# Kernel optimization log

Measured on AMD Instinct MI355X. Metric: run time of the kernel, lower is better.

## Reference

```python
import jax, jax.numpy as jnp
import numpy as np

N = 50000      # nodes
E = 800000     # edges (avg degree 16)
DIN = 500      # input_dim
HID = 100      # hid_dim (fixed in module)
DOUT = 64      # output_dim
EPS = 1e-5     # LayerNorm eps (torch default)


def _layer_norm(x, g, b):
    mu = jnp.mean(x, axis=-1, keepdims=True)
    var = jnp.var(x, axis=-1, keepdims=True)
    return (x - mu) / jnp.sqrt(var + EPS) * g + b


def _gcn_conv(x, src, tgt, W, b):
    # PyG GCNConv: self-loops + symmetric normalization + linear + scatter-add
    h = x @ W  # [N, out]
    idx = jnp.arange(N)
    src_sl = jnp.concatenate([src, idx])
    tgt_sl = jnp.concatenate([tgt, idx])
    deg = jax.ops.segment_sum(jnp.ones(src_sl.shape, h.dtype), tgt_sl, num_segments=N)
    dinv = jnp.where(deg > 0, deg ** -0.5, 0.0)
    norm = dinv[src_sl] * dinv[tgt_sl]  # [E+N]
    out = jax.ops.segment_sum(h[src_sl] * norm[:, None], tgt_sl, num_segments=N)
    return out + b


def setup_inputs() -> dict:
    key = jax.random.key(0)
    ks = jax.random.split(key, 10)
    glorot = lambda k, fi, fo: jax.random.normal(k, (fi, fo), jnp.float32) * np.float32(1.0 / np.sqrt(fi))
    z = lambda d: jnp.zeros((d,), jnp.float32)
    return dict(
        data_x=jax.random.normal(ks[0], (N, DIN), jnp.float32),
        data_edge_index=jax.random.randint(ks[1], (2, E), 0, N),
        data_edge_attr=jnp.zeros((E,), jnp.int32),  # single relation type
        t_W1=glorot(ks[2], DIN, HID), t_b1=z(HID), t_g1=jnp.ones((HID,), jnp.float32), t_be1=z(HID),
        t_W2=glorot(ks[3], HID, HID), t_b2=z(HID), t_g2=jnp.ones((HID,), jnp.float32), t_be2=z(HID),
        r_Wrel=glorot(ks[4], HID, HID)[None],  # [n_relations=1, H, H]
        r_Wself=glorot(ks[5], HID, HID), r_b=z(HID),
        c1_W=glorot(ks[6], HID, HID), c1_b=z(HID),
        c2_W=glorot(ks[7], HID, DOUT), c2_b=z(DOUT),
    )


def reference(data_x, data_edge_index, data_edge_attr,
              t_W1, t_b1, t_g1, t_be1, t_W2, t_b2, t_g2, t_be2,
              r_Wrel, r_Wself, r_b, c1_W, c1_b, c2_W, c2_b):
    src, tgt = data_edge_index[0], data_edge_index[1]
    # transform: Linear -> LN -> ReLU -> Linear -> LN -> ReLU
    x = jax.nn.relu(_layer_norm(data_x @ t_W1 + t_b1, t_g1, t_be1))
    x = jax.nn.relu(_layer_norm(x @ t_W2 + t_b2, t_g2, t_be2))
    # RGCN, n_relations=1, n_layers=1: per-relation message + self transform
    msgs = x[src] @ r_Wrel[0]  # edge_attr is all relation 0
    x = x @ r_Wself + jax.ops.segment_sum(msgs, tgt, num_segments=N) + r_b
    x = jax.nn.relu(x)  # dropout = identity (eval)
    x = jax.nn.relu(_gcn_conv(x, src, tgt, c1_W, c1_b))
    x = _gcn_conv(x, src, tgt, c2_W, c2_b)
    return jax.nn.log_softmax(x, axis=1)
```

## Files before the change

kernel.cpp:

```cpp
#include <hip/hip_runtime.h>
#include <hip/hip_bf16.h>

typedef __attribute__((ext_vector_type(8))) short short8;
typedef __attribute__((ext_vector_type(8))) unsigned short ushort8;
typedef __attribute__((ext_vector_type(4))) float f32x4;

static constexpr int NN = 50000;
static constexpr int NE = 800000;
static constexpr int SCAN_B = 196;

#define MFMA16x16x32 __builtin_amdgcn_mfma_f32_16x16x32_bf16

__device__ __forceinline__ float b2f(unsigned short u){
  unsigned v = ((unsigned)u) << 16;
  return __builtin_bit_cast(float, v);
}
__device__ __forceinline__ unsigned short f2b(float f){
  unsigned x = __builtin_bit_cast(unsigned, f);
  unsigned r = (x + 0x7fffu + ((x >> 16) & 1u)) >> 16;
  return (unsigned short)r;
}

__device__ __align__(256) int   g_isf32;
__device__ __align__(256) unsigned short g_W1t  [112 * 512];
__device__ __align__(256) unsigned short g_W2t  [112 * 128];
__device__ __align__(256) unsigned short g_WselfT[112 * 128];
__device__ __align__(256) unsigned short g_WrelT [112 * 128];
__device__ __align__(256) unsigned short g_c1Wt [112 * 128];
__device__ __align__(256) unsigned short g_c2Wt [64 * 128];
__device__ __align__(256) unsigned short g_bufA[(size_t)NN * 128];
__device__ __align__(256) unsigned short g_bufB[(size_t)NN * 128];
__device__ __align__(256) unsigned short g_bufC[(size_t)NN * 128];
__device__ __align__(256) int   g_deg[NN];
__device__ __align__(256) int   g_rowptr[NN + 1];
__device__ __align__(256) int   g_cursor[NN];
__device__ __align__(256) int   g_colidx[NE];
__device__ __align__(256) float g_dinv[NN];
__device__ __align__(256) int   g_partial[256];

__device__ __forceinline__ float ld_in(const void* p, int idx, int isf32){
  if (isf32) return ((const float*)p)[idx];
  return b2f(((const unsigned short*)p)[idx]);
}

__global__ void k_detect(const unsigned short* __restrict__ x){
  __shared__ int sh[256];
  int tid = threadIdx.x;
  int cnt = 0;
  for (int j = 0; j < 16; j++){
    unsigned short h = x[(size_t)(tid * 16 + j) * 2];
    int e = (h >> 7) & 0xFF;
    if (e >= 90 && e <= 160) cnt++;
  }
  sh[tid] = cnt;
  __syncthreads();
  for (int off = 128; off > 0; off >>= 1){
    if (tid < off) sh[tid] += sh[tid + off];
    __syncthreads();
  }
  if (tid == 0) g_isf32 = (sh[0] < 2458) ? 1 : 0;
}

__global__ void k_zero(){
  int i = blockIdx.x * 256 + threadIdx.x;
  if (i < NN){ g_deg[i] = 0; g_cursor[i] = 0; }
}

__device__ __forceinline__ void xp_one(const void* W, unsigned short* Wt, int idx,
                                       int K, int Nc, int Kpad, int isf32){
  int n = idx / Kpad;
  int k = idx - n * Kpad;
  float v = 0.f;
  if (n < Nc && k < K) v = ld_in(W, k * Nc + n, isf32);
  Wt[idx] = f2b(v);
}
__global__ void k_transpose_all(const void* W1, const void* W2, const void* Wself,
                                const void* Wrel, const void* c1W, const void* c2W){
  int idx = blockIdx.x * 256 + threadIdx.x;
  const int isf32 = g_isf32;
  if (idx < 57344){ xp_one(W1, g_W1t, idx, 500, 100, 512, isf32); return; }
  idx -= 57344;
  if (idx < 14336){ xp_one(W2,    g_W2t,    idx, 100, 100, 128, isf32); return; }
  idx -= 14336;
  if (idx < 14336){ xp_one(Wself, g_WselfT, idx, 100, 100, 128, isf32); return; }
  idx -= 14336;
  if (idx < 14336){ xp_one(Wrel,  g_WrelT,  idx, 100, 100, 128, isf32); return; }
  idx -= 14336;
  if (idx < 14336){ xp_one(c1W,   g_c1Wt,   idx, 100, 100, 128, isf32); return; }
  idx -= 14336;
  if (idx < 8192){  xp_one(c2W,   g_c2Wt,   idx, 100, 64,  128, isf32); }
}

__global__ void k_deg(const int* __restrict__ tgt){
  int e = blockIdx.x * 256 + threadIdx.x;
  if (e < NE) atomicAdd(&g_deg[tgt[e]], 1);
}

__global__ __launch_bounds__(256) void k_scan1(){
  __shared__ int sh[256];
  int t = threadIdx.x;
  int i = blockIdx.x * 256 + t;
  int val = (i < NN) ? g_deg[i] : 0;
  sh[t] = val;
  __syncthreads();
#pragma unroll
  for (int off = 1; off < 256; off <<= 1){
    int v = (t >= off) ? sh[t - off] : 0;
    __syncthreads();
    sh[t] += v;
    __syncthreads();
  }
  if (i < NN){
    g_rowptr[i] = sh[t] - val;
    g_dinv[i] = rsqrtf((float)(val + 1));
  }
  if (t == 255) g_partial[blockIdx.x] = sh[255];
}
__global__ __launch_bounds__(256) void k_scan2(){
  __shared__ int sh[256];
  int t = threadIdx.x;
  int val = (t < SCAN_B) ? g_partial[t] : 0;
  sh[t] = val;
  __syncthreads();
#pragma unroll
  for (int off = 1; off < 256; off <<= 1){
    int v = (t >= off) ? sh[t - off] : 0;
    __syncthreads();
    sh[t] += v;
    __syncthreads();
  }
  if (t < SCAN_B) g_partial[t] = sh[t] - val;
  if (t == 255) g_rowptr[NN] = sh[255];
}
__global__ __launch_bounds__(256) void k_scan3(){
  int i = blockIdx.x * 256 + threadIdx.x;
  if (i < NN) g_rowptr[i] += g_partial[blockIdx.x];
}

__global__ void k_fill(const int* __restrict__ src, const int* __restrict__ tgt){
  int e = blockIdx.x * 256 + threadIdx.x;
  if (e >= NE) return;
  int t = tgt[e];
  int pos = g_rowptr[t] + atomicAdd(&g_cursor[t], 1);
  g_colidx[pos] = src[e];
}

template<int MODE>
__global__ __launch_bounds__(256) void k_agg(){
  const unsigned short* x = (MODE == 1) ? g_bufC : g_bufB;
  int node = blockIdx.x * 16 + (threadIdx.x >> 4);
  if (node >= NN) return;
  const int c8 = (threadIdx.x & 15) * 8;

  float wt = (MODE != 0) ? g_dinv[node] : 1.f;
  float a[4][8];
#pragma unroll
  for (int j = 0; j < 4; j++)
#pragma unroll
    for (int k = 0; k < 8; k++) a[j][k] = 0.f;

  int p0 = g_rowptr[node], p1 = g_rowptr[node + 1];
  for (int p = p0; p < p1; p += 4){
    int   sj[4]; float wj[4];
#pragma unroll
    for (int j = 0; j < 4; j++){
      bool ok = (p + j) < p1;
      sj[j] = ok ? g_colidx[p + j] : node;
      wj[j] = ok ? ((MODE != 0) ? g_dinv[sj[j]] * wt : 1.f) : 0.f;
    }
    ushort8 r[4];
#pragma unroll
    for (int j = 0; j < 4; j++)
      r[j] = *reinterpret_cast<const ushort8*>(&x[(size_t)sj[j] * 128 + c8]);
#pragma unroll
    for (int j = 0; j < 4; j++)
#pragma unroll
      for (int k = 0; k < 8; k++) a[j][k] += wj[j] * b2f((unsigned short)r[j][k]);
  }
  if (MODE != 0){
    float ws = wt * wt;
    ushort8 sv = *reinterpret_cast<const ushort8*>(&x[(size_t)node * 128 + c8]);
#pragma unroll
    for (int k = 0; k < 8; k++) a[0][k] += ws * b2f((unsigned short)sv[k]);
  }
  ushort8 o;
#pragma unroll
  for (int k = 0; k < 8; k++)
    o[k] = f2b(a[0][k] + a[1][k] + a[2][k] + a[3][k]);
  *reinterpret_cast<ushort8*>(&g_bufA[(size_t)node * 128 + c8]) = o;
}

__global__ __launch_bounds__(64, 1) void k_gemm1_ln(const void* __restrict__ Aext,
    const void* __restrict__ bias, const void* __restrict__ gamma,
    const void* __restrict__ beta){
  const int lane = threadIdx.x;
  const int m = lane & 15, q = lane >> 4;
  const int row0 = blockIdx.x * 16;
  const int isf32 = g_isf32;
  f32x4 acc[7] = {};

  if (isf32){
    const float* arow = (const float*)Aext + (size_t)(row0 + m) * 500;
    const int kq = q * 8;
    f32x4 lo = *reinterpret_cast<const f32x4*>(arow + min(kq, 496));
    f32x4 hi = *reinterpret_cast<const f32x4*>(arow + min(kq + 4, 496));
#pragma unroll
    for (int c = 0; c < 16; c++){
      f32x4 lo2 = lo, hi2 = hi;
      if (c < 15){
        int kn = (c + 1) * 32 + kq;
        lo2 = *reinterpret_cast<const f32x4*>(arow + min(kn, 496));
        hi2 = *reinterpret_cast<const f32x4*>(arow + min(kn + 4, 496));
      }
      short8 a = {(short)f2b(lo[0]), (short)f2b(lo[1]), (short)f2b(lo[2]), (short)f2b(lo[3]),
                  (short)f2b(hi[0]), (short)f2b(hi[1]), (short)f2b(hi[2]), (short)f2b(hi[3])};
      const int k0 = c * 32 + kq;
#pragma unroll
      for (int t = 0; t < 7; t++){
        short8 b = *reinterpret_cast<const short8*>(g_W1t + (size_t)(t * 16 + m) * 512 + k0);
        acc[t] = MFMA16x16x32(a, b, acc[t], 0, 0, 0);
      }
      lo = lo2; hi = hi2;
    }
  } else {
    const unsigned short* arow = (const unsigned short*)Aext + (size_t)(row0 + m) * 500;
    const int kq = q * 8;
    ushort4 lo = *reinterpret_cast<const ushort4*>(arow + min(kq, 496));
    ushort4 hi = *reinterpret_cast<const ushort4*>(arow + min(kq + 4, 496));
#pragma unroll
    for (int c = 0; c < 16; c++){
      ushort4 lo2 = lo, hi2 = hi;
      if (c < 15){
        int kn = (c + 1) * 32 + kq;
        lo2 = *reinterpret_cast<const ushort4*>(arow + min(kn, 496));
        hi2 = *reinterpret_cast<const ushort4*>(arow + min(kn + 4, 496));
      }
      short8 a = {(short)lo.x, (short)lo.y, (short)lo.z, (short)lo.w,
                  (short)hi.x, (short)hi.y, (short)hi.z, (short)hi.w};
      const int k0 = c * 32 + kq;
#pragma unroll
      for (int t = 0; t < 7; t++){
        short8 b = *reinterpret_cast<const short8*>(g_W1t + (size_t)(t * 16 + m) * 512 + k0);
        acc[t] = MFMA16x16x32(a, b, acc[t], 0, 0, 0);
      }
      lo = lo2; hi = hi2;
    }
  }

  float bf_[7], gf_[7], ef_[7];
#pragma unroll
  for (int t = 0; t < 7; t++){
    int col = t * 16 + m;
    bool ok = col < 100;
    bf_[t] = ok ? ld_in(bias, col, isf32)  : 0.f;
    gf_[t] = ok ? ld_in(gamma, col, isf32) : 0.f;
    ef_[t] = ok ? ld_in(beta, col, isf32)  : 0.f;
  }
#pragma unroll
  for (int r = 0; r < 4; r++){
    float vals[7], s1 = 0.f, s2 = 0.f;
#pragma unroll
    for (int t = 0; t < 7; t++){
      int col = t * 16 + m;
      float v = (col < 100) ? (acc[t][r] + bf_[t]) : 0.f;
      vals[t] = v; s1 += v; s2 += v * v;
    }
#pragma unroll
    for (int msk = 1; msk < 16; msk <<= 1){
      s1 += __shfl_xor(s1, msk, 64);
      s2 += __shfl_xor(s2, msk, 64);
    }
    float mu = s1 * 0.01f;
    float var = fmaxf(s2 * 0.01f - mu * mu, 0.f);
    float rstd = rsqrtf(var + 1e-5f);
    unsigned short* orow = g_bufA + (size_t)(row0 + q * 4 + r) * 128;
#pragma unroll
    for (int t = 0; t < 7; t++){
      int col = t * 16 + m;
      float y = fmaxf((vals[t] - mu) * rstd * gf_[t] + ef_[t], 0.f);
      orow[col] = f2b((col < 100) ? y : 0.f);
    }
    orow[112 + m] = 0;
  }
}

__global__ __launch_bounds__(256) void k_gemm2_ln(const void* __restrict__ bias,
    const void* __restrict__ gamma, const void* __restrict__ beta){
  const int isf32 = g_isf32;
  const int wave = threadIdx.x >> 6, lane = threadIdx.x & 63;
  const int m = lane & 15, q = lane >> 4;
  const int row0 = (blockIdx.x * 4 + wave) * 16;
  if (row0 >= NN) return;
  f32x4 acc[7] = {};
  const unsigned short* arow = g_bufA + (size_t)(row0 + m) * 128;
#pragma unroll
  for (int c = 0; c < 4; c++){
    const int k0 = c * 32 + q * 8;
    short8 a = *reinterpret_cast<const short8*>(arow + k0);
#pragma unroll
    for (int t = 0; t < 7; t++){
      short8 b = *reinterpret_cast<const short8*>(g_W2t + (size_t)(t * 16 + m) * 128 + k0);
      acc[t] = MFMA16x16x32(a, b, acc[t], 0, 0, 0);
    }
  }
  float bf_[7], gf_[7], ef_[7];
#pragma unroll
  for (int t = 0; t < 7; t++){
    int col = t * 16 + m;
    bool ok = col < 100;
    bf_[t] = ok ? ld_in(bias, col, isf32)  : 0.f;
    gf_[t] = ok ? ld_in(gamma, col, isf32) : 0.f;
    ef_[t] = ok ? ld_in(beta, col, isf32)  : 0.f;
  }
#pragma unroll
  for (int r = 0; r < 4; r++){
    float vals[7], s1 = 0.f, s2 = 0.f;
#pragma unroll
    for (int t = 0; t < 7; t++){
      int col = t * 16 + m;
      float v = (col < 100) ? (acc[t][r] + bf_[t]) : 0.f;
      vals[t] = v; s1 += v; s2 += v * v;
    }
#pragma unroll
    for (int msk = 1; msk < 16; msk <<= 1){
      s1 += __shfl_xor(s1, msk, 64);
      s2 += __shfl_xor(s2, msk, 64);
    }
    float mu = s1 * 0.01f;
    float var = fmaxf(s2 * 0.01f - mu * mu, 0.f);
    float rstd = rsqrtf(var + 1e-5f);
    unsigned short* orow = g_bufB + (size_t)(row0 + q * 4 + r) * 128;
#pragma unroll
    for (int t = 0; t < 7; t++){
      int col = t * 16 + m;
      float y = fmaxf((vals[t] - mu) * rstd * gf_[t] + ef_[t], 0.f);
      orow[col] = f2b((col < 100) ? y : 0.f);
    }
    orow[112 + m] = 0;
  }
}

template<int SEL>
__global__ __launch_bounds__(256) void k_gemm_bias_relu(const void* __restrict__ bias){
  const unsigned short* A1  = (SEL == 0) ? g_bufB : g_bufA;
  const unsigned short* B1t = (SEL == 0) ? g_WselfT : g_c1Wt;
  unsigned short* out       = (SEL == 0) ? g_bufC : g_bufB;
  const int isf32 = g_isf32;

  const int wave = threadIdx.x >> 6, lane = threadIdx.x & 63;
  const int m = lane & 15, q = lane >> 4;
  const int row0 = (blockIdx.x * 4 + wave) * 16;
  if (row0 >= NN) return;
  f32x4 acc[7] = {};
  const unsigned short* a1row = A1 + (size_t)(row0 + m) * 128;
#pragma unroll
  for (int c = 0; c < 4; c++){
    const int k0 = c * 32 + q * 8;
    short8 a = *reinterpret_cast<const short8*>(a1row + k0);
#pragma unroll
    for (int t = 0; t < 7; t++){
      short8 b = *reinterpret_cast<const short8*>(B1t + (size_t)(t * 16 + m) * 128 + k0);
      acc[t] = MFMA16x16x32(a, b, acc[t], 0, 0, 0);
    }
  }
  if (SEL == 0){
    const unsigned short* a2row = g_bufA + (size_t)(row0 + m) * 128;
#pragma unroll
    for (int c = 0; c < 4; c++){
      const int k0 = c * 32 + q * 8;
      short8 a = *reinterpret_cast<const short8*>(a2row + k0);
#pragma unroll
      for (int t = 0; t < 7; t++){
        short8 b = *reinterpret_cast<const short8*>(g_WrelT + (size_t)(t * 16 + m) * 128 + k0);
        acc[t] = MFMA16x16x32(a, b, acc[t], 0, 0, 0);
      }
    }
  }
  float bf_[7];
#pragma unroll
  for (int t = 0; t < 7; t++){
    int col = t * 16 + m;
    bf_[t] = (col < 100) ? ld_in(bias, col, isf32) : 0.f;
  }
#pragma unroll
  for (int r = 0; r < 4; r++){
    unsigned short* orow = out + (size_t)(row0 + q * 4 + r) * 128;
#pragma unroll
    for (int t = 0; t < 7; t++){
      int col = t * 16 + m;
      float y = fmaxf(acc[t][r] + bf_[t], 0.f);
      orow[col] = f2b((col < 100) ? y : 0.f);
    }
    orow[112 + m] = 0;
  }
}

__global__ __launch_bounds__(256) void k_gemm_lsm(const void* __restrict__ bias,
                                                  void* __restrict__ outv){
  const int isf32 = g_isf32;
  const int wave = threadIdx.x >> 6, lane = threadIdx.x & 63;
  const int m = lane & 15, q = lane >> 4;
  const int row0 = (blockIdx.x * 4 + wave) * 16;
  if (row0 >= NN) return;
  f32x4 acc[4] = {};
  const unsigned short* arow = g_bufA + (size_t)(row0 + m) * 128;
#pragma unroll
  for (int c = 0; c < 4; c++){
    const int k0 = c * 32 + q * 8;
    short8 a = *reinterpret_cast<const short8*>(arow + k0);
#pragma unroll
    for (int t = 0; t < 4; t++){
      short8 b = *reinterpret_cast<const short8*>(g_c2Wt + (size_t)(t * 16 + m) * 128 + k0);
      acc[t] = MFMA16x16x32(a, b, acc[t], 0, 0, 0);
    }
  }
  float bf_[4];
#pragma unroll
  for (int t = 0; t < 4; t++) bf_[t] = ld_in(bias, t * 16 + m, isf32);
#pragma unroll
  for (int r = 0; r < 4; r++){
    float vals[4], mx = -1e30f;
#pragma unroll
    for (int t = 0; t < 4; t++){
      float v = acc[t][r] + bf_[t];
      vals[t] = v; mx = fmaxf(mx, v);
    }
#pragma unroll
    for (int msk = 1; msk < 16; msk <<= 1) mx = fmaxf(mx, __shfl_xor(mx, msk, 64));
    float se = 0.f;
#pragma unroll
    for (int t = 0; t < 4; t++) se += expf(vals[t] - mx);
#pragma unroll
    for (int msk = 1; msk < 16; msk <<= 1) se += __shfl_xor(se, msk, 64);
    float lse = logf(se);
    size_t ro = (size_t)(row0 + q * 4 + r) * 64;
    if (isf32){
      float* orow = (float*)outv + ro;
#pragma unroll
      for (int t = 0; t < 4; t++) orow[t * 16 + m] = vals[t] - mx - lse;
    } else {
      unsigned short* orow = (unsigned short*)outv + ro;
#pragma unroll
      for (int t = 0; t < 4; t++) orow[t * 16 + m] = f2b(vals[t] - mx - lse);
    }
  }
}

extern "C" void kernel_launch(void* const* d_in, const int* in_sizes, int n_in,
                              void* d_out, int out_size, void* d_ws, size_t ws_size,
                              hipStream_t stream){
  (void)in_sizes; (void)n_in; (void)out_size; (void)d_ws; (void)ws_size;
  const void* data_x = d_in[0];
  const int* ei = (const int*)d_in[1];
  const int* src = ei;
  const int* tgt = ei + NE;
  const void *W1 = d_in[3], *b1 = d_in[4], *gm1 = d_in[5], *be1 = d_in[6];
  const void *W2 = d_in[7], *b2 = d_in[8], *gm2 = d_in[9], *be2 = d_in[10];
  const void *Wrel = d_in[11], *Wself = d_in[12], *rb = d_in[13];
  const void *c1W = d_in[14], *c1b = d_in[15];
  const void *c2W = d_in[16], *c2b = d_in[17];

  k_detect<<<1, 256, 0, stream>>>((const unsigned short*)data_x);
  k_zero<<<(NN + 255) / 256, 256, 0, stream>>>();
  k_transpose_all<<<(122880 + 255) / 256, 256, 0, stream>>>(W1, W2, Wself, Wrel, c1W, c2W);

  k_deg<<<(NE + 255) / 256, 256, 0, stream>>>(tgt);
  k_scan1<<<SCAN_B, 256, 0, stream>>>();
  k_scan2<<<1, 256, 0, stream>>>();
  k_scan3<<<SCAN_B, 256, 0, stream>>>();
  k_fill<<<(NE + 255) / 256, 256, 0, stream>>>(src, tgt);

  const int G64 = (NN + 63) / 64;
  const int GA  = (NN + 15) / 16;
  k_gemm1_ln<<<3125, 64, 0, stream>>>(data_x, b1, gm1, be1);
  k_gemm2_ln<<<G64, 256, 0, stream>>>(b2, gm2, be2);
  k_agg<0><<<GA, 256, 0, stream>>>();
  k_gemm_bias_relu<0><<<G64, 256, 0, stream>>>(rb);
  k_agg<1><<<GA, 256, 0, stream>>>();
  k_gemm_bias_relu<1><<<G64, 256, 0, stream>>>(c1b);
  k_agg<2><<<GA, 256, 0, stream>>>();
  k_gemm_lsm<<<G64, 256, 0, stream>>>(c2b, d_out);
}
```

Baseline: 520.8 us.

## Stage fp32 input rows into LDS via async global_load_lds double buffering

In the first GEMM+LayerNorm kernel, the fp32 input path now loads 16 rows of X in 128-column chunks with global_load_lds into a double-buffered shared array. The next chunk is prefetched while MFMAs run on the current one. This replaces per-lane strided global loads with coalesced row-contiguous loads and raw vmcnt waits. The bf16 path loses its register prefetch and becomes a simple load loop. The hardcoded waitcnt encodings and min-clamped tail columns add correctness risk.

```diff
diff --git a/kernel.cpp b/kernel.cpp
--- a/kernel.cpp
+++ b/kernel.cpp
@@ -19,6 +19,12 @@
   unsigned x = __builtin_bit_cast(unsigned, f);
   unsigned r = (x + 0x7fffu + ((x >> 16) & 1u)) >> 16;
   return (unsigned short)r;
+}
+
+__device__ __forceinline__ void gld16(const void* g, void* l){
+  __builtin_amdgcn_global_load_lds(
+      (const __attribute__((address_space(1))) void*)g,
+      (__attribute__((address_space(3))) void*)l, 16, 0, 0);
 }
 
 __device__ __align__(256) int   g_isf32;
@@ -193,6 +199,7 @@
 __global__ __launch_bounds__(64, 1) void k_gemm1_ln(const void* __restrict__ Aext,
     const void* __restrict__ bias, const void* __restrict__ gamma,
     const void* __restrict__ beta){
+  __shared__ float sA[2][2048];
   const int lane = threadIdx.x;
   const int m = lane & 15, q = lane >> 4;
   const int row0 = blockIdx.x * 16;
@@ -200,50 +207,56 @@
   f32x4 acc[7] = {};
 
   if (isf32){
-    const float* arow = (const float*)Aext + (size_t)(row0 + m) * 500;
-    const int kq = q * 8;
-    f32x4 lo = *reinterpret_cast<const f32x4*>(arow + min(kq, 496));
-    f32x4 hi = *reinterpret_cast<const f32x4*>(arow + min(kq + 4, 496));
-#pragma unroll
-    for (int c = 0; c < 16; c++){
-      f32x4 lo2 = lo, hi2 = hi;
-      if (c < 15){
-        int kn = (c + 1) * 32 + kq;
-        lo2 = *reinterpret_cast<const f32x4*>(arow + min(kn, 496));
-        hi2 = *reinterpret_cast<const f32x4*>(arow + min(kn + 4, 496));
+    const float* X = (const float*)Aext;
+    const int jr = lane >> 5;
+    const int cg = (lane & 31) * 4;
+#pragma unroll
+    for (int j = 0; j < 8; j++)
+      gld16(X + (size_t)(row0 + 2 * j + jr) * 500 + min(cg, 496), &sA[0][j * 256]);
+#pragma unroll
+    for (int kc = 0; kc < 4; kc++){
+      if (kc < 3){
+        const int gc = (kc + 1) * 128 + cg;
+#pragma unroll
+        for (int j = 0; j < 8; j++)
+          gld16(X + (size_t)(row0 + 2 * j + jr) * 500 + min(gc, 496),
+                &sA[(kc + 1) & 1][j * 256]);
+        __builtin_amdgcn_s_waitcnt(0x0F78);
+      } else {
+        __builtin_amdgcn_s_waitcnt(0x0F70);
       }
-      short8 a = {(short)f2b(lo[0]), (short)f2b(lo[1]), (short)f2b(lo[2]), (short)f2b(lo[3]),
-                  (short)f2b(hi[0]), (short)f2b(hi[1]), (short)f2b(hi[2]), (short)f2b(hi[3])};
-      const int k0 = c * 32 + kq;
-#pragma unroll
-      for (int t = 0; t < 7; t++){
-        short8 b = *reinterpret_cast<const short8*>(g_W1t + (size_t)(t * 16 + m) * 512 + k0);
-        acc[t] = MFMA16x16x32(a, b, acc[t], 0, 0, 0);
+      const float* sb = sA[kc & 1];
+      const int ridx = (m >> 1) * 256 + (m & 1) * 128;
+#pragma unroll
+      for (int c = 0; c < 4; c++){
+        const int kq = c * 32 + q * 8;
+        f32x4 lo = *reinterpret_cast<const f32x4*>(sb + ridx + kq);
+        f32x4 hi = *reinterpret_cast<const f32x4*>(sb + ridx + kq + 4);
+        short8 a = {(short)f2b(lo[0]), (short)f2b(lo[1]), (short)f2b(lo[2]), (short)f2b(lo[3]),
+                    (short)f2b(hi[0]), (short)f2b(hi[1]), (short)f2b(hi[2]), (short)f2b(hi[3])};
+        const int k0 = kc * 128 + kq;
+#pragma unroll
+        for (int t = 0; t < 7; t++){
+          short8 b = *reinterpret_cast<const short8*>(g_W1t + (size_t)(t * 16 + m) * 512 + k0);
+          acc[t] = MFMA16x16x32(a, b, acc[t], 0, 0, 0);
+        }
       }
-      lo = lo2; hi = hi2;
     }
   } else {
     const unsigned short* arow = (const unsigned short*)Aext + (size_t)(row0 + m) * 500;
     const int kq = q * 8;
-    ushort4 lo = *reinterpret_cast<const ushort4*>(arow + min(kq, 496));
-    ushort4 hi = *reinterpret_cast<const ushort4*>(arow + min(kq + 4, 496));
 #pragma unroll
     for (int c = 0; c < 16; c++){
-      ushort4 lo2 = lo, hi2 = hi;
-      if (c < 15){
-        int kn = (c + 1) * 32 + kq;
-        lo2 = *reinterpret_cast<const ushort4*>(arow + min(kn, 496));
-        hi2 = *reinterpret_cast<const ushort4*>(arow + min(kn + 4, 496));
-      }
+      int kb = c * 32 + kq;
+      ushort4 lo = *reinterpret_cast<const ushort4*>(arow + min(kb, 496));
+      ushort4 hi = *reinterpret_cast<const ushort4*>(arow + min(kb + 4, 496));
       short8 a = {(short)lo.x, (short)lo.y, (short)lo.z, (short)lo.w,
                   (short)hi.x, (short)hi.y, (short)hi.z, (short)hi.w};
-      const int k0 = c * 32 + kq;
 #pragma unroll
       for (int t = 0; t < 7; t++){
-        short8 b = *reinterpret_cast<const short8*>(g_W1t + (size_t)(t * 16 + m) * 512 + k0);
+        short8 b = *reinterpret_cast<const short8*>(g_W1t + (size_t)(t * 16 + m) * 512 + kb);
         acc[t] = MFMA16x16x32(a, b, acc[t], 0, 0, 0);
       }
-      lo = lo2; hi = hi2;
     }
   }
 
```

After: 528.6 us. No clear change (+1.5%).

## Split-K first GEMM across four waves and reorder last GCN as transform-then-aggregate

Applied to the files above, without the earlier changes.

The first GEMM kernel now uses four waves per 16-row block. Each wave handles a quarter of the K dimension, and the partial sums are reduced through shared memory before the LayerNorm epilogue. The final GCN layer now multiplies by c2_W first, producing 64-wide rows in a new buffer. A fused aggregation plus log-softmax kernel then gathers over those narrower rows, so the gather moves half as many bytes per edge. The trade-offs are a 28KB shared-memory reduction with a barrier, three idle waves during the epilogue, and reliance on g_bufB/g_bufC buffers that must already exist and hold the expected data.

```diff
diff --git a/kernel.cpp b/kernel.cpp
--- a/kernel.cpp
+++ b/kernel.cpp
@@ -190,62 +190,69 @@
   *reinterpret_cast<ushort8*>(&g_bufA[(size_t)node * 128 + c8]) = o;
 }
 
-__global__ __launch_bounds__(64, 1) void k_gemm1_ln(const void* __restrict__ Aext,
+__global__ __launch_bounds__(256, 4) void k_gemm1_ln(const void* __restrict__ Aext,
     const void* __restrict__ bias, const void* __restrict__ gamma,
     const void* __restrict__ beta){
-  const int lane = threadIdx.x;
+  __shared__ float red[28 * 256];
+  const int tid = threadIdx.x;
+  const int w = tid >> 6, lane = tid & 63;
   const int m = lane & 15, q = lane >> 4;
   const int row0 = blockIdx.x * 16;
   const int isf32 = g_isf32;
+  const int kbase = w * 128;
   f32x4 acc[7] = {};
 
   if (isf32){
-    const float* arow = (const float*)Aext + (size_t)(row0 + m) * 500;
-    const int kq = q * 8;
-    f32x4 lo = *reinterpret_cast<const f32x4*>(arow + min(kq, 496));
-    f32x4 hi = *reinterpret_cast<const f32x4*>(arow + min(kq + 4, 496));
-#pragma unroll
-    for (int c = 0; c < 16; c++){
-      f32x4 lo2 = lo, hi2 = hi;
-      if (c < 15){
-        int kn = (c + 1) * 32 + kq;
-        lo2 = *reinterpret_cast<const f32x4*>(arow + min(kn, 496));
-        hi2 = *reinterpret_cast<const f32x4*>(arow + min(kn + 4, 496));
-      }
+    const float* base = (const float*)Aext + (size_t)(row0 + m) * 500;
+    f32x4 L[8];
+#pragma unroll
+    for (int c = 0; c < 4; c++){
+      int col = kbase + c * 32 + q * 8;
+      L[2 * c]     = *reinterpret_cast<const f32x4*>(base + min(col, 496));
+      L[2 * c + 1] = *reinterpret_cast<const f32x4*>(base + min(col + 4, 496));
+    }
+#pragma unroll
+    for (int c = 0; c < 4; c++){
+      f32x4 lo = L[2 * c], hi = L[2 * c + 1];
       short8 a = {(short)f2b(lo[0]), (short)f2b(lo[1]), (short)f2b(lo[2]), (short)f2b(lo[3]),
                   (short)f2b(hi[0]), (short)f2b(hi[1]), (short)f2b(hi[2]), (short)f2b(hi[3])};
-      const int k0 = c * 32 + kq;
+      const int k0 = kbase + c * 32 + q * 8;
 #pragma unroll
       for (int t = 0; t < 7; t++){
         short8 b = *reinterpret_cast<const short8*>(g_W1t + (size_t)(t * 16 + m) * 512 + k0);
         acc[t] = MFMA16x16x32(a, b, acc[t], 0, 0, 0);
       }
-      lo = lo2; hi = hi2;
     }
   } else {
-    const unsigned short* arow = (const unsigned short*)Aext + (size_t)(row0 + m) * 500;
-    const int kq = q * 8;
-    ushort4 lo = *reinterpret_cast<const ushort4*>(arow + min(kq, 496));
-    ushort4 hi = *reinterpret_cast<const ushort4*>(arow + min(kq + 4, 496));
-#pragma unroll
-    for (int c = 0; c < 16; c++){
-      ushort4 lo2 = lo, hi2 = hi;
-      if (c < 15){
-        int kn = (c + 1) * 32 + kq;
-        lo2 = *reinterpret_cast<const ushort4*>(arow + min(kn, 496));
-        hi2 = *reinterpret_cast<const ushort4*>(arow + min(kn + 4, 496));
-      }
+    const unsigned short* base = (const unsigned short*)Aext + (size_t)(row0 + m) * 500;
+    ushort4 U[8];
+#pragma unroll
+    for (int c = 0; c < 4; c++){
+      int col = kbase + c * 32 + q * 8;
+      U[2 * c]     = *reinterpret_cast<const ushort4*>(base + min(col, 496));
+      U[2 * c + 1] = *reinterpret_cast<const ushort4*>(base + min(col + 4, 496));
+    }
+#pragma unroll
+    for (int c = 0; c < 4; c++){
+      ushort4 lo = U[2 * c], hi = U[2 * c + 1];
       short8 a = {(short)lo.x, (short)lo.y, (short)lo.z, (short)lo.w,
                   (short)hi.x, (short)hi.y, (short)hi.z, (short)hi.w};
-      const int k0 = c * 32 + kq;
+      const int k0 = kbase + c * 32 + q * 8;
 #pragma unroll
       for (int t = 0; t < 7; t++){
         short8 b = *reinterpret_cast<const short8*>(g_W1t + (size_t)(t * 16 + m) * 512 + k0);
         acc[t] = MFMA16x16x32(a, b, acc[t], 0, 0, 0);
       }
-      lo = lo2; hi = hi2;
-    }
-  }
+    }
+  }
+
+#pragma unroll
+  for (int t = 0; t < 7; t++)
+#pragma unroll
+    for (int r = 0; r < 4; r++)
+      red[(t * 4 + r) * 256 + tid] = acc[t][r];
+  __syncthreads();
+  if (w != 0) return;
 
   float bf_[7], gf_[7], ef_[7];
 #pragma unroll
@@ -261,8 +268,10 @@
     float vals[7], s1 = 0.f, s2 = 0.f;
 #pragma unroll
     for (int t = 0; t < 7; t++){
+      const float* rv = &red[(t * 4 + r) * 256];
+      float v = rv[lane] + rv[64 + lane] + rv[128 + lane] + rv[192 + lane];
       int col = t * 16 + m;
-      float v = (col < 100) ? (acc[t][r] + bf_[t]) : 0.f;
+      v = (col < 100) ? (v + bf_[t]) : 0.f;
       vals[t] = v; s1 += v; s2 += v * v;
     }
 #pragma unroll
@@ -395,15 +404,13 @@
   }
 }
 
-__global__ __launch_bounds__(256) void k_gemm_lsm(const void* __restrict__ bias,
-                                                  void* __restrict__ outv){
-  const int isf32 = g_isf32;
+__global__ __launch_bounds__(256) void k_gemm_c2(){
   const int wave = threadIdx.x >> 6, lane = threadIdx.x & 63;
   const int m = lane & 15, q = lane >> 4;
   const int row0 = (blockIdx.x * 4 + wave) * 16;
   if (row0 >= NN) return;
   f32x4 acc[4] = {};
-  const unsigned short* arow = g_bufA + (size_t)(row0 + m) * 128;
+  const unsigned short* arow = g_bufB + (size_t)(row0 + m) * 128;
 #pragma unroll
   for (int c = 0; c < 4; c++){
     const int k0 = c * 32 + q * 8;
@@ -414,35 +421,73 @@
       acc[t] = MFMA16x16x32(a, b, acc[t], 0, 0, 0);
     }
   }
-  float bf_[4];
-#pragma unroll
-  for (int t = 0; t < 4; t++) bf_[t] = ld_in(bias, t * 16 + m, isf32);
 #pragma unroll
   for (int r = 0; r < 4; r++){
-    float vals[4], mx = -1e30f;
-#pragma unroll
-    for (int t = 0; t < 4; t++){
-      float v = acc[t][r] + bf_[t];
-      vals[t] = v; mx = fmaxf(mx, v);
-    }
-#pragma unroll
-    for (int msk = 1; msk < 16; msk <<= 1) mx = fmaxf(mx, __shfl_xor(mx, msk, 64));
-    float se = 0.f;
-#pragma unroll
-    for (int t = 0; t < 4; t++) se += expf(vals[t] - mx);
-#pragma unroll
-    for (int msk = 1; msk < 16; msk <<= 1) se += __shfl_xor(se, msk, 64);
-    float lse = logf(se);
-    size_t ro = (size_t)(row0 + q * 4 + r) * 64;
-    if (isf32){
-      float* orow = (float*)outv + ro;
-#pragma unroll
-      for (int t = 0; t < 4; t++) orow[t * 16 + m] = vals[t] - mx - lse;
-    } else {
-      unsigned short* orow = (unsigned short*)outv + ro;
-#pragma unroll
-      for (int t = 0; t < 4; t++) orow[t * 16 + m] = f2b(vals[t] - mx - lse);
-    }
+    unsigned short* orow = g_bufC + (size_t)(row0 + q * 4 + r) * 64;
+#pragma unroll
+    for (int t = 0; t < 4; t++) orow[t * 16 + m] = f2b(acc[t][r]);
+  }
+}
+
+__global__ __launch_bounds__(256) void k_agg_lsm(const void* __restrict__ bias,
+                                                 void* __restrict__ outv){
+  const int isf32 = g_isf32;
+  int node = blockIdx.x * 32 + (threadIdx.x >> 3);
+  if (node >= NN) return;
+  const int c8 = (threadIdx.x & 7) * 8;
+  float wt = g_dinv[node];
+  float a[4][8];
+#pragma unroll
+  for (int j = 0; j < 4; j++)
+#pragma unroll
+    for (int k = 0; k < 8; k++) a[j][k] = 0.f;
+
+  int p0 = g_rowptr[node], p1 = g_rowptr[node + 1];
+  for (int p = p0; p < p1; p += 4){
+    int   sj[4]; float wj[4];
+#pragma unroll
+    for (int j = 0; j < 4; j++){
+      bool ok = (p + j) < p1;
+      sj[j] = ok ? g_colidx[p + j] : node;
+      wj[j] = ok ? g_dinv[sj[j]] * wt : 0.f;
+    }
+    ushort8 r[4];
+#pragma unroll
+    for (int j = 0; j < 4; j++)
+      r[j] = *reinterpret_cast<const ushort8*>(&g_bufC[(size_t)sj[j] * 64 + c8]);
+#pragma unroll
+    for (int j = 0; j < 4; j++)
+#pragma unroll
+      for (int k = 0; k < 8; k++) a[j][k] += wj[j] * b2f((unsigned short)r[j][k]);
+  }
+  float ws = wt * wt;
+  ushort8 sv = *reinterpret_cast<const ushort8*>(&g_bufC[(size_t)node * 64 + c8]);
+#pragma unroll
+  for (int k = 0; k < 8; k++) a[0][k] += ws * b2f((unsigned short)sv[k]);
+
+  float v[8], mx = -1e30f;
+#pragma unroll
+  for (int k = 0; k < 8; k++){
+    v[k] = a[0][k] + a[1][k] + a[2][k] + a[3][k] + ld_in(bias, c8 + k, isf32);
+    mx = fmaxf(mx, v[k]);
+  }
+#pragma unroll
+  for (int msk = 1; msk < 8; msk <<= 1) mx = fmaxf(mx, __shfl_xor(mx, msk, 64));
+  float se = 0.f;
+#pragma unroll
+  for (int k = 0; k < 8; k++) se += expf(v[k] - mx);
+#pragma unroll
+  for (int msk = 1; msk < 8; msk <<= 1) se += __shfl_xor(se, msk, 64);
+  float lse = logf(se);
+  size_t ro = (size_t)node * 64 + c8;
+  if (isf32){
+    float* o = (float*)outv + ro;
+#pragma unroll
+    for (int k = 0; k < 8; k++) o[k] = v[k] - mx - lse;
+  } else {
+    unsigned short* o = (unsigned short*)outv + ro;
+#pragma unroll
+    for (int k = 0; k < 8; k++) o[k] = f2b(v[k] - mx - lse);
   }
 }
 
@@ -472,12 +517,12 @@
 
   const int G64 = (NN + 63) / 64;
   const int GA  = (NN + 15) / 16;
-  k_gemm1_ln<<<3125, 64, 0, stream>>>(data_x, b1, gm1, be1);
+  k_gemm1_ln<<<3125, 256, 0, stream>>>(data_x, b1, gm1, be1);
   k_gemm2_ln<<<G64, 256, 0, stream>>>(b2, gm2, be2);
   k_agg<0><<<GA, 256, 0, stream>>>();
   k_gemm_bias_relu<0><<<G64, 256, 0, stream>>>(rb);
   k_agg<1><<<GA, 256, 0, stream>>>();
   k_gemm_bias_relu<1><<<G64, 256, 0, stream>>>(c1b);
-  k_agg<2><<<GA, 256, 0, stream>>>();
-  k_gemm_lsm<<<G64, 256, 0, stream>>>(c2b, d_out);
-}
+  k_gemm_c2<<<G64, 256, 0, stream>>>();
+  k_agg_lsm<<<(NN + 31) / 32, 256, 0, stream>>>(c2b, d_out);
+}
```

Result: faster. 507.1 us (-2.6%).
